# Optimization experiments

Hardware: AMD Instinct MI355X
Metric: run time of the kernel (lower is better)

The kernel has to match this reference:

```python
import jax, jax.numpy as jnp
import numpy as np

# db4 analysis filters (pywt.Wavelet('db4').dec_lo / dec_hi)
_DEC_LO = np.array([-0.010597401784997278, 0.032883011666982945, 0.030841381835986965,
                    -0.18703481171888114, -0.02798376941698385, 0.6308807679295904,
                    0.7148465705525415, 0.23037781330885523], dtype=np.float32)
_DEC_HI = np.array([-0.23037781330885523, 0.7148465705525415, -0.6308807679295904,
                    -0.02798376941698385, 0.18703481171888114, 0.030841381835986965,
                    -0.032883011666982945, -0.010597401784997278], dtype=np.float32)
# pytorch_wavelets stores filters reversed (torch conv = correlation); lax.conv is
# also correlation, so use the same reversed filters. Shape [2, 1, L].
_H = jnp.asarray(np.stack([_DEC_LO[::-1], _DEC_HI[::-1]])[:, None, :])

B, SW, SWS, HW, K, J = 2048, 4, 64, 8, 128, 3
DWT_LEN = 84  # 14 (lo, level 3) + 35 (hi1) + 21 (hi2) + 14 (hi3)


def _dwt_level(x, h):
    """One analysis level, mode='reflect' (pytorch_wavelets afb1d). x: [M, N]."""
    N = x.shape[-1]
    L = h.shape[-1]
    outsize = (N + L - 1) // 2          # pywt.dwt_coeff_len, non-periodization
    p = 2 * (outsize - 1) - N + L
    if p % 2 == 1:                       # odd total pad: one extra zero at the end
        x = jnp.pad(x, ((0, 0), (0, 1)))
    x = jnp.pad(x, ((0, 0), (p // 2, p // 2)), mode='reflect')
    y = jax.lax.conv_general_dilated(x[:, None, :], h, (2,), 'VALID')  # [M, 2, out]
    return y[:, 0, :], y[:, 1, :]


def setup_inputs() -> dict:
    key = jax.random.key(0)
    k1, k2, k3 = jax.random.split(key, 3)
    x = jax.random.normal(k1, (B, 1, SW * SWS, HW, HW), dtype=jnp.float32)
    # one Conv3d(1 -> K, kernel=(DWT_LEN, 8, 8)) per subwindow, kaiming-ish init
    fan_in = DWT_LEN * HW * HW
    conv_weight = jax.random.normal(k2, (SW, K, DWT_LEN, HW, HW), dtype=jnp.float32) / np.sqrt(fan_in)
    conv_bias = jax.random.normal(k3, (SW, K), dtype=jnp.float32) * 0.01
    return {"x": x, "conv_weight": conv_weight, "conv_bias": conv_bias}


def reference(x, conv_weight, conv_bias):
    b = x.shape[0]
    # [B,1,T,8,8] -> [B,SW,8,8,SWS]: DWT runs along the time axis of each subwindow
    xt = x[:, 0].reshape(b, SW, SWS, HW, HW).transpose(0, 1, 3, 4, 2)
    xm = xt.reshape(-1, SWS)  # [B*SW*64, 64]
    lo, highs = xm, []
    for _ in range(J):
        lo, hi = _dwt_level(lo, _H)
        highs.append(hi)
    coeffs = jnp.concatenate([lo] + highs, axis=-1)  # [M, 84], order: lo, hi1, hi2, hi3
    c = coeffs.reshape(b, SW, HW, HW, DWT_LEN).transpose(0, 1, 4, 2, 3)  # [B,SW,84,8,8]
    # per-subwindow Conv3d that fully reduces (t,h,w) -> [B, SW, K]
    feat = jnp.einsum('bsthw,skthw->bsk', c, conv_weight) + conv_bias[None]
    # Dropout3d is identity in eval; LeakyReLU default slope 0.01 (typo in source
    # means leakyrelu_negative_slope is never applied)
    return jax.nn.leaky_relu(feat, 0.01).reshape(b, SW * K)
```

## Files before the change

kernel.cpp:

```cpp
#include <hip/hip_runtime.h>
#include <stdint.h>

typedef unsigned int  u32;
typedef unsigned short u16;
typedef __bf16 bf16x8 __attribute__((ext_vector_type(8)));
typedef float  f32x4  __attribute__((ext_vector_type(4)));
typedef u32    u32x4  __attribute__((ext_vector_type(4)));

__constant__ float GL[8] = { 0.23037781330885523f,  0.7148465705525415f,
                             0.6308807679295904f,  -0.02798376941698385f,
                            -0.18703481171888114f,  0.030841381835986965f,
                             0.032883011666982945f,-0.010597401784997278f };
__constant__ float GH[8] = {-0.010597401784997278f,-0.032883011666982945f,
                             0.030841381835986965f, 0.18703481171888114f,
                            -0.02798376941698385f, -0.6308807679295904f,
                             0.7148465705525415f,  -0.23037781330885523f };

__device__ inline u16 f32_bf16(float f) {
    u32 u = __float_as_uint(f);
    u += 0x7fffu + ((u >> 16) & 1u);
    return (u16)(u >> 16);
}
__device__ inline u32 pack2_bf16(float a, float b) {
    u32 ua = __float_as_uint(a); ua += 0x7fffu + ((ua >> 16) & 1u);
    u32 ub = __float_as_uint(b); ub += 0x7fffu + ((ub >> 16) & 1u);
    return (ua >> 16) | (ub & 0xffff0000u);
}

__global__ __launch_bounds__(256) void fold_w(const float* __restrict__ cw,
                                              u16* __restrict__ Wf) {
    __shared__ float WdL[84 * 64];
    const int tid = threadIdx.x;

    if (tid < 64) {
        const int j = tid;
        float lo1[35], lo2[21];
#pragma unroll
        for (int i = 0; i < 35; ++i) {
            float sl = 0.f, sh = 0.f;
#pragma unroll
            for (int t = 0; t < 8; ++t) {
                int s = 2 * i + t - 6;
                if (s < 0) s = -s;
                if (s >= 64) s = 126 - s;
                float xv = (s == j) ? 1.0f : 0.0f;
                sl += xv * GL[t]; sh += xv * GH[t];
            }
            lo1[i] = sl;
            WdL[(14 + i) * 64 + j] = sh;
        }
#pragma unroll
        for (int i = 0; i < 21; ++i) {
            float sl = 0.f, sh = 0.f;
#pragma unroll
            for (int t = 0; t < 8; ++t) {
                int s = 2 * i + t - 6;
                if (s < 0) s = -s;
                if (s >= 36) s = 70 - s;
                float xv = (s >= 35) ? 0.0f : lo1[s];
                sl += xv * GL[t]; sh += xv * GH[t];
            }
            lo2[i] = sl;
            WdL[(49 + i) * 64 + j] = sh;
        }
#pragma unroll
        for (int i = 0; i < 14; ++i) {
            float sl = 0.f, sh = 0.f;
#pragma unroll
            for (int t = 0; t < 8; ++t) {
                int s = 2 * i + t - 6;
                if (s < 0) s = -s;
                if (s >= 22) s = 42 - s;
                float xv = (s >= 21) ? 0.0f : lo2[s];
                sl += xv * GL[t]; sh += xv * GH[t];
            }
            WdL[i * 64 + j] = sl;
            WdL[(70 + i) * 64 + j] = sh;
        }
    }
    __syncthreads();

    const int sk = blockIdx.x;
    const int s  = sk >> 7;
    const int n  = sk & 127;
    const int hw = tid & 63;
    const int tg = __builtin_amdgcn_readfirstlane((int)(tid >> 6));
    const int t0 = tg * 16;
    const float* wk = cw + (size_t)sk * (84 * 64);
    float acc[16];
#pragma unroll
    for (int j = 0; j < 16; ++j) acc[j] = 0.f;
#pragma unroll 4
    for (int tau = 0; tau < 84; ++tau) {
        float wv = wk[tau * 64 + hw];
        const float* Wr = WdL + tau * 64 + t0;
#pragma unroll
        for (int j = 0; j < 16; ++j) acc[j] += wv * Wr[j];
    }
    const int nt = n >> 4;
    const int fr = n & 15;
    const int fq = (hw >> 3) & 3;
    const int jj = hw & 7;
    const int kbh = hw >> 5;
#pragma unroll
    for (int j = 0; j < 16; ++j) {
        const int t = t0 + j;
        const size_t idx =
            ((((size_t)(s * 8 + nt)) * 128 + t * 2 + kbh) * 64 + fq * 16 + fr) * 8 + jj;
        Wf[idx] = f32_bf16(acc[j]);
    }
}

template <int NKB>
__global__ __launch_bounds__(256, 3) void gemm2(const float* __restrict__ X,
                                                const u16* __restrict__ Wf,
                                                float* __restrict__ P) {
    const int tid  = threadIdx.x;
    const int lane = tid & 63;
    const int gw   = blockIdx.x * 4 + (tid >> 6);
    const int ksid = gw >> 9;
    const int rem  = gw & 511;
    const int s    = rem >> 7;
    const int mt   = rem & 127;
    const int fr   = lane & 15;
    const int fq   = lane >> 4;
    const int kb0  = ksid * NKB;

    const float* xg = X + (size_t)(mt * 16 + fr) * 16384 + s * 4096 + kb0 * 32 + fq * 8;
    const u16*   wg = Wf + (((size_t)(s * 8) * 128) + kb0) * 512 + lane * 8;

    f32x4 acc[8];
#pragma unroll
    for (int nt = 0; nt < 8; ++nt) acc[nt] = (f32x4){0.f, 0.f, 0.f, 0.f};

    f32x4 a0 = __builtin_nontemporal_load(reinterpret_cast<const f32x4*>(xg));
    f32x4 a1 = __builtin_nontemporal_load(reinterpret_cast<const f32x4*>(xg) + 1);

#pragma unroll 2
    for (int kb = 0; kb < NKB; ++kb) {
        union { u32 u[4]; bf16x8 v; } av;
        av.u[0] = pack2_bf16(a0.x, a0.y); av.u[1] = pack2_bf16(a0.z, a0.w);
        av.u[2] = pack2_bf16(a1.x, a1.y); av.u[3] = pack2_bf16(a1.z, a1.w);
        const int kn = (kb + 1 < NKB) ? kb + 1 : kb;
        a0 = __builtin_nontemporal_load(reinterpret_cast<const f32x4*>(xg + (size_t)kn * 32));
        a1 = __builtin_nontemporal_load(reinterpret_cast<const f32x4*>(xg + (size_t)kn * 32) + 1);
        const u16* wb = wg + (size_t)kb * 512;
#pragma unroll
        for (int nt = 0; nt < 8; ++nt) {
            bf16x8 bf = *reinterpret_cast<const bf16x8*>(wb + (size_t)nt * 65536);
            acc[nt] = __builtin_amdgcn_mfma_f32_16x16x32_bf16(av.v, bf, acc[nt], 0, 0, 0);
        }
    }

    float* pg = P + (size_t)ksid * (2048 * 512) + (size_t)(mt * 16) * 512 + s * 128 + fr;
#pragma unroll
    for (int nt = 0; nt < 8; ++nt)
#pragma unroll
        for (int r = 0; r < 4; ++r)
            __builtin_nontemporal_store(acc[nt][r], pg + (size_t)(fq * 4 + r) * 512 + nt * 16);
}

__global__ __launch_bounds__(256) void reduce_k(const float* __restrict__ P,
                                                const float* __restrict__ bias,
                                                float* __restrict__ out, int nks) {
    const int t = blockIdx.x * 256 + threadIdx.x;
    const size_t base = (size_t)t * 4;
    f32x4 sum = {0.f, 0.f, 0.f, 0.f};
    for (int k = 0; k < nks; ++k) {
        f32x4 v = __builtin_nontemporal_load(
            reinterpret_cast<const f32x4*>(P + (size_t)k * (2048 * 512) + base));
        sum += v;
    }
    const f32x4 b = *reinterpret_cast<const f32x4*>(bias + (base & 511));
    f32x4 o = sum + b;
    o.x = o.x > 0.f ? o.x : 0.01f * o.x;
    o.y = o.y > 0.f ? o.y : 0.01f * o.y;
    o.z = o.z > 0.f ? o.z : 0.01f * o.z;
    o.w = o.w > 0.f ? o.w : 0.01f * o.w;
    __builtin_nontemporal_store(o, reinterpret_cast<f32x4*>(out + base));
}

extern "C" void kernel_launch(void* const* d_in, const int* in_sizes, int n_in,
                              void* d_out, int out_size, void* d_ws, size_t ws_size,
                              hipStream_t stream) {
    const float* x  = (const float*)d_in[0];
    const float* cw = (const float*)d_in[1];
    const float* cb = (const float*)d_in[2];
    float* out = (float*)d_out;

    u16*   Wf = (u16*)d_ws;
    float* P  = (float*)((char*)d_ws + (4u << 20));

    const size_t MN = (size_t)2048 * 512 * 4;
    int ks = (ws_size >= (4u << 20) + 8 * MN) ? 8
           : (ws_size >= (4u << 20) + 4 * MN) ? 4
           : (ws_size >= (4u << 20) + 2 * MN) ? 2 : 1;

    fold_w<<<512, 256, 0, stream>>>(cw, Wf);
    switch (ks) {
        case 8: gemm2<16> <<<128 * 8, 256, 0, stream>>>(x, Wf, P); break;
        case 4: gemm2<32> <<<128 * 4, 256, 0, stream>>>(x, Wf, P); break;
        case 2: gemm2<64> <<<128 * 2, 256, 0, stream>>>(x, Wf, P); break;
        default: gemm2<128><<<128 * 1, 256, 0, stream>>>(x, Wf, P); break;
    }
    reduce_k<<<1024, 256, 0, stream>>>(P, cb, out, ks);
}
```

Measured before the change: 245.4 us.

## Fuse split-K reduction into GEMM via LDS atomics and precompute DWT matrix at compile time

The separate reduce kernel and the global partial-sum buffer are removed. Each 512-thread block now has 8 waves, each covering a different K slice, and their partials are summed in shared memory with atomics before bias and LeakyReLU are applied in-kernel. The DWT analysis matrix is built as a constexpr constant table, so the per-block shared-memory construction in fold_w goes away. This saves the global round trip for partials and one launch, at the cost of LDS atomic contention and fewer, larger blocks.

Measured after the change: 272.4 us. 1.11x slower.

```diff
diff --git a/kernel.cpp b/kernel.cpp
--- a/kernel.cpp
+++ b/kernel.cpp
@@ -1,20 +1,60 @@
 #include <hip/hip_runtime.h>
 #include <stdint.h>
 
-typedef unsigned int  u32;
+typedef unsigned int   u32;
 typedef unsigned short u16;
 typedef __bf16 bf16x8 __attribute__((ext_vector_type(8)));
 typedef float  f32x4  __attribute__((ext_vector_type(4)));
-typedef u32    u32x4  __attribute__((ext_vector_type(4)));
 
-__constant__ float GL[8] = { 0.23037781330885523f,  0.7148465705525415f,
-                             0.6308807679295904f,  -0.02798376941698385f,
-                            -0.18703481171888114f,  0.030841381835986965f,
-                             0.032883011666982945f,-0.010597401784997278f };
-__constant__ float GH[8] = {-0.010597401784997278f,-0.032883011666982945f,
-                             0.030841381835986965f, 0.18703481171888114f,
-                            -0.02798376941698385f, -0.6308807679295904f,
-                             0.7148465705525415f,  -0.23037781330885523f };
+struct WdT { float v[84][64]; };
+
+constexpr WdT build_wd() {
+    WdT W{};
+    const float GLc[8] = { 0.23037781330885523f,  0.7148465705525415f,
+                           0.6308807679295904f,  -0.02798376941698385f,
+                          -0.18703481171888114f,  0.030841381835986965f,
+                           0.032883011666982945f,-0.010597401784997278f };
+    const float GHc[8] = {-0.010597401784997278f,-0.032883011666982945f,
+                           0.030841381835986965f, 0.18703481171888114f,
+                          -0.02798376941698385f, -0.6308807679295904f,
+                           0.7148465705525415f,  -0.23037781330885523f };
+    for (int j = 0; j < 64; ++j) {
+        float lo1[35] = {}, lo2[21] = {};
+        for (int i = 0; i < 35; ++i) {
+            float sl = 0.f, sh = 0.f;
+            for (int t = 0; t < 8; ++t) {
+                int s = 2*i + t - 6;
+                if (s < 0)   s = -s;
+                if (s >= 64) s = 126 - s;
+                if (s == j) { sl += GLc[t]; sh += GHc[t]; }
+            }
+            lo1[i] = sl; W.v[14 + i][j] = sh;
+        }
+        for (int i = 0; i < 21; ++i) {
+            float sl = 0.f, sh = 0.f;
+            for (int t = 0; t < 8; ++t) {
+                int s = 2*i + t - 6;
+                if (s < 0)   s = -s;
+                if (s >= 36) s = 70 - s;
+                if (s < 35) { sl += lo1[s]*GLc[t]; sh += lo1[s]*GHc[t]; }
+            }
+            lo2[i] = sl; W.v[49 + i][j] = sh;
+        }
+        for (int i = 0; i < 14; ++i) {
+            float sl = 0.f, sh = 0.f;
+            for (int t = 0; t < 8; ++t) {
+                int s = 2*i + t - 6;
+                if (s < 0)   s = -s;
+                if (s >= 22) s = 42 - s;
+                if (s < 21) { sl += lo2[s]*GLc[t]; sh += lo2[s]*GHc[t]; }
+            }
+            W.v[i][j] = sl; W.v[70 + i][j] = sh;
+        }
+    }
+    return W;
+}
+
+__constant__ WdT WD = build_wd();
 
 __device__ inline u16 f32_bf16(float f) {
     u32 u = __float_as_uint(f);
@@ -29,78 +69,30 @@
 
 __global__ __launch_bounds__(256) void fold_w(const float* __restrict__ cw,
                                               u16* __restrict__ Wf) {
-    __shared__ float WdL[84 * 64];
     const int tid = threadIdx.x;
+    const int sk  = blockIdx.x;
+    const int s   = sk >> 7;
+    const int n   = sk & 127;
+    const int hw  = tid & 63;
+    const int tg  = __builtin_amdgcn_readfirstlane((int)(tid >> 6));
+    const int t0  = tg * 16;
+    const float* wk = cw + (size_t)sk * (84 * 64);
 
-    if (tid < 64) {
-        const int j = tid;
-        float lo1[35], lo2[21];
-#pragma unroll
-        for (int i = 0; i < 35; ++i) {
-            float sl = 0.f, sh = 0.f;
-#pragma unroll
-            for (int t = 0; t < 8; ++t) {
-                int s = 2 * i + t - 6;
-                if (s < 0) s = -s;
-                if (s >= 64) s = 126 - s;
-                float xv = (s == j) ? 1.0f : 0.0f;
-                sl += xv * GL[t]; sh += xv * GH[t];
-            }
-            lo1[i] = sl;
-            WdL[(14 + i) * 64 + j] = sh;
-        }
-#pragma unroll
-        for (int i = 0; i < 21; ++i) {
-            float sl = 0.f, sh = 0.f;
-#pragma unroll
-            for (int t = 0; t < 8; ++t) {
-                int s = 2 * i + t - 6;
-                if (s < 0) s = -s;
-                if (s >= 36) s = 70 - s;
-                float xv = (s >= 35) ? 0.0f : lo1[s];
-                sl += xv * GL[t]; sh += xv * GH[t];
-            }
-            lo2[i] = sl;
-            WdL[(49 + i) * 64 + j] = sh;
-        }
-#pragma unroll
-        for (int i = 0; i < 14; ++i) {
-            float sl = 0.f, sh = 0.f;
-#pragma unroll
-            for (int t = 0; t < 8; ++t) {
-                int s = 2 * i + t - 6;
-                if (s < 0) s = -s;
-                if (s >= 22) s = 42 - s;
-                float xv = (s >= 21) ? 0.0f : lo2[s];
-                sl += xv * GL[t]; sh += xv * GH[t];
-            }
-            WdL[i * 64 + j] = sl;
-            WdL[(70 + i) * 64 + j] = sh;
-        }
-    }
-    __syncthreads();
-
-    const int sk = blockIdx.x;
-    const int s  = sk >> 7;
-    const int n  = sk & 127;
-    const int hw = tid & 63;
-    const int tg = __builtin_amdgcn_readfirstlane((int)(tid >> 6));
-    const int t0 = tg * 16;
-    const float* wk = cw + (size_t)sk * (84 * 64);
     float acc[16];
 #pragma unroll
     for (int j = 0; j < 16; ++j) acc[j] = 0.f;
+
 #pragma unroll 4
     for (int tau = 0; tau < 84; ++tau) {
-        float wv = wk[tau * 64 + hw];
-        const float* Wr = WdL + tau * 64 + t0;
+        const float wv = wk[tau * 64 + hw];
 #pragma unroll
-        for (int j = 0; j < 16; ++j) acc[j] += wv * Wr[j];
+        for (int j = 0; j < 16; ++j) acc[j] += wv * WD.v[tau][t0 + j];
     }
-    const int nt = n >> 4;
-    const int fr = n & 15;
-    const int fq = (hw >> 3) & 3;
-    const int jj = hw & 7;
+
+    const int nt  = n >> 4;
+    const int fr  = n & 15;
+    const int fq  = (hw >> 3) & 3;
+    const int jj  = hw & 7;
     const int kbh = hw >> 5;
 #pragma unroll
     for (int j = 0; j < 16; ++j) {
@@ -111,23 +103,24 @@
     }
 }
 
-template <int NKB>
-__global__ __launch_bounds__(256, 3) void gemm2(const float* __restrict__ X,
-                                                const u16* __restrict__ Wf,
-                                                float* __restrict__ P) {
+__global__ __launch_bounds__(512, 4) void gemm_f(const float* __restrict__ X,
+                                                 const u16* __restrict__ Wf,
+                                                 const float* __restrict__ bias,
+                                                 float* __restrict__ out) {
+    __shared__ __align__(16) float R[16 * 132];
     const int tid  = threadIdx.x;
     const int lane = tid & 63;
-    const int gw   = blockIdx.x * 4 + (tid >> 6);
-    const int ksid = gw >> 9;
-    const int rem  = gw & 511;
-    const int s    = rem >> 7;
-    const int mt   = rem & 127;
+    const int w    = tid >> 6;
+    const int s    = blockIdx.x >> 7;
+    const int mt   = blockIdx.x & 127;
     const int fr   = lane & 15;
     const int fq   = lane >> 4;
-    const int kb0  = ksid * NKB;
+    const int kb0  = w * 16;
+
+    for (int i = tid; i < 16 * 132; i += 512) R[i] = 0.f;
 
     const float* xg = X + (size_t)(mt * 16 + fr) * 16384 + s * 4096 + kb0 * 32 + fq * 8;
-    const u16*   wg = Wf + (((size_t)(s * 8) * 128) + kb0) * 512 + lane * 8;
+    const u16*   wg = Wf + ((size_t)(s * 8) * 128 + kb0) * 512 + lane * 8;
 
     f32x4 acc[8];
 #pragma unroll
@@ -136,12 +129,14 @@
     f32x4 a0 = __builtin_nontemporal_load(reinterpret_cast<const f32x4*>(xg));
     f32x4 a1 = __builtin_nontemporal_load(reinterpret_cast<const f32x4*>(xg) + 1);
 
+    __syncthreads();
+
 #pragma unroll 2
-    for (int kb = 0; kb < NKB; ++kb) {
+    for (int kb = 0; kb < 16; ++kb) {
         union { u32 u[4]; bf16x8 v; } av;
         av.u[0] = pack2_bf16(a0.x, a0.y); av.u[1] = pack2_bf16(a0.z, a0.w);
         av.u[2] = pack2_bf16(a1.x, a1.y); av.u[3] = pack2_bf16(a1.z, a1.w);
-        const int kn = (kb + 1 < NKB) ? kb + 1 : kb;
+        const int kn = (kb + 1 < 16) ? kb + 1 : kb;
         a0 = __builtin_nontemporal_load(reinterpret_cast<const f32x4*>(xg + (size_t)kn * 32));
         a1 = __builtin_nontemporal_load(reinterpret_cast<const f32x4*>(xg + (size_t)kn * 32) + 1);
         const u16* wb = wg + (size_t)kb * 512;
@@ -152,32 +147,27 @@
         }
     }
 
-    float* pg = P + (size_t)ksid * (2048 * 512) + (size_t)(mt * 16) * 512 + s * 128 + fr;
 #pragma unroll
     for (int nt = 0; nt < 8; ++nt)
 #pragma unroll
         for (int r = 0; r < 4; ++r)
-            __builtin_nontemporal_store(acc[nt][r], pg + (size_t)(fq * 4 + r) * 512 + nt * 16);
-}
+            atomicAdd(&R[(fq * 4 + r) * 132 + nt * 16 + fr], acc[nt][r]);
+    __syncthreads();
 
-__global__ __launch_bounds__(256) void reduce_k(const float* __restrict__ P,
-                                                const float* __restrict__ bias,
-                                                float* __restrict__ out, int nks) {
-    const int t = blockIdx.x * 256 + threadIdx.x;
-    const size_t base = (size_t)t * 4;
-    f32x4 sum = {0.f, 0.f, 0.f, 0.f};
-    for (int k = 0; k < nks; ++k) {
-        f32x4 v = __builtin_nontemporal_load(
-            reinterpret_cast<const f32x4*>(P + (size_t)k * (2048 * 512) + base));
-        sum += v;
+    {
+        const int o   = tid * 4;
+        const int row = o >> 7;
+        const int col = o & 127;
+        f32x4 v = *reinterpret_cast<const f32x4*>(&R[row * 132 + col]);
+        const f32x4 b = *reinterpret_cast<const f32x4*>(bias + s * 128 + col);
+        f32x4 u = v + b;
+        u.x = u.x > 0.f ? u.x : 0.01f * u.x;
+        u.y = u.y > 0.f ? u.y : 0.01f * u.y;
+        u.z = u.z > 0.f ? u.z : 0.01f * u.z;
+        u.w = u.w > 0.f ? u.w : 0.01f * u.w;
+        __builtin_nontemporal_store(
+            u, reinterpret_cast<f32x4*>(out + (size_t)(mt * 16 + row) * 512 + s * 128 + col));
     }
-    const f32x4 b = *reinterpret_cast<const f32x4*>(bias + (base & 511));
-    f32x4 o = sum + b;
-    o.x = o.x > 0.f ? o.x : 0.01f * o.x;
-    o.y = o.y > 0.f ? o.y : 0.01f * o.y;
-    o.z = o.z > 0.f ? o.z : 0.01f * o.z;
-    o.w = o.w > 0.f ? o.w : 0.01f * o.w;
-    __builtin_nontemporal_store(o, reinterpret_cast<f32x4*>(out + base));
 }
 
 extern "C" void kernel_launch(void* const* d_in, const int* in_sizes, int n_in,
@@ -188,20 +178,8 @@
     const float* cb = (const float*)d_in[2];
     float* out = (float*)d_out;
 
-    u16*   Wf = (u16*)d_ws;
-    float* P  = (float*)((char*)d_ws + (4u << 20));
-
-    const size_t MN = (size_t)2048 * 512 * 4;
-    int ks = (ws_size >= (4u << 20) + 8 * MN) ? 8
-           : (ws_size >= (4u << 20) + 4 * MN) ? 4
-           : (ws_size >= (4u << 20) + 2 * MN) ? 2 : 1;
+    u16* Wf = (u16*)d_ws;
 
     fold_w<<<512, 256, 0, stream>>>(cw, Wf);
-    switch (ks) {
-        case 8: gemm2<16> <<<128 * 8, 256, 0, stream>>>(x, Wf, P); break;
-        case 4: gemm2<32> <<<128 * 4, 256, 0, stream>>>(x, Wf, P); break;
-        case 2: gemm2<64> <<<128 * 2, 256, 0, stream>>>(x, Wf, P); break;
-        default: gemm2<128><<<128 * 1, 256, 0, stream>>>(x, Wf, P); break;
-    }
-    reduce_k<<<1024, 256, 0, stream>>>(P, cb, out, ks);
+    gemm_f<<<512, 512, 0, stream>>>(x, Wf, cb, out);
 }
```
